# Kernel optimization log

Measured on AMD Instinct MI355X. Metric: run time of the kernel, lower is better.

## Reference

```python
import jax, jax.numpy as jnp
import numpy as np

N, DIN, DOUT = 8192, 256, 128
NEG_SLOPE = 0.01         # F.leaky_relu default
MASK_VAL = -9.0e15       # from the torch source


def setup_inputs() -> dict:
    key = jax.random.key(0)
    kx, kadj, kW, kbW, ka1, ka2, kba = jax.random.split(key, 7)
    x = jax.random.normal(kx, (N, DIN), dtype=jnp.float32)
    adj = jax.random.randint(kadj, (N, N), 0, 2, dtype=jnp.int32)
    # Linear W: input_dim -> output_dim
    W = jax.random.normal(kW, (DIN, DOUT), dtype=jnp.float32) * (1.0 / np.sqrt(DIN))
    bW = jax.random.normal(kbW, (DOUT,), dtype=jnp.float32) * 0.01
    # Linear a: 2*output_dim -> 1, split into the h_i part (a1) and h_j part (a2)
    a1 = jax.random.normal(ka1, (DOUT,), dtype=jnp.float32) * (1.0 / np.sqrt(2 * DOUT))
    a2 = jax.random.normal(ka2, (DOUT,), dtype=jnp.float32) * (1.0 / np.sqrt(2 * DOUT))
    ba = jax.random.normal(kba, (), dtype=jnp.float32) * 0.01
    return {"x": x, "adj": adj, "W": W, "bW": bW, "a1": a1, "a2": a2, "ba": ba}


def reference(x, adj, W, bW, a1, a2, ba):
    # h = W x + b  -> [N, DOUT]
    h = x @ W + bW
    # e[i,j] = leaky_relu(a . [h_i, h_j] + ba) = leaky_relu(a1.h_i + a2.h_j + ba)
    s_src = h @ a1            # [N]
    s_dst = h @ a2            # [N]
    e = s_src[:, None] + s_dst[None, :] + ba   # [N, N]
    e = jnp.where(e > 0, e, NEG_SLOPE * e)
    # mask non-edges, row softmax over neighbors j
    e = jnp.where(adj > 0, e, MASK_VAL)
    alpha = jax.nn.softmax(e, axis=1)          # [N, N]
    # dropout is identity in eval mode (dropout_rate=0)
    return alpha @ h                            # [N, DOUT]
```

## Files before the change

kernel.cpp:

```cpp
#include <hip/hip_runtime.h>
#include <hip/hip_bf16.h>


#define NN 8192
#define DIN 256
#define DOUT 128
#define LOG2E 1.4426950408889634f

typedef __attribute__((ext_vector_type(8))) short short8;
typedef __attribute__((ext_vector_type(4))) float floatx4;

__global__ void prep_wt(const float* __restrict__ W, __hip_bfloat16* __restrict__ WT) {
    int e = blockIdx.x * blockDim.x + threadIdx.x;
    if (e < DIN * DOUT) {
        int k = e >> 7;
        int d = e & 127;
        WT[d * DIN + k] = __float2bfloat16(W[e]);
    }
}

__global__ __launch_bounds__(256, 4) void gat_h(
    const float* __restrict__ x, const __hip_bfloat16* __restrict__ WT,
    const float* __restrict__ bW, const float* __restrict__ a1, const float* __restrict__ a2,
    __hip_bfloat16* __restrict__ hbT, float* __restrict__ s_src, float* __restrict__ s_dst) {
    int tid = threadIdx.x;
    int w = tid >> 6, lane = tid & 63;
    int lm = lane & 15, lq = lane >> 4;
    int i0 = blockIdx.x * 32;
    int r0 = (w >> 1) * 16;
    int c0 = (w & 1) * 64;

    __shared__ float s1s[32], s2s[32];
    if (tid < 32) { s1s[tid] = 0.f; s2s[tid] = 0.f; }
    __syncthreads();

    floatx4 acc[4] = {};
#pragma unroll
    for (int kk = 0; kk < DIN; kk += 32) {
        const float4* xp = (const float4*)&x[(size_t)(i0 + r0 + lm) * DIN + kk + lq * 8];
        float4 xa = xp[0], xb = xp[1];
        union { short8 v; __hip_bfloat16 h[8]; } af;
        af.h[0] = __float2bfloat16(xa.x); af.h[1] = __float2bfloat16(xa.y);
        af.h[2] = __float2bfloat16(xa.z); af.h[3] = __float2bfloat16(xa.w);
        af.h[4] = __float2bfloat16(xb.x); af.h[5] = __float2bfloat16(xb.y);
        af.h[6] = __float2bfloat16(xb.z); af.h[7] = __float2bfloat16(xb.w);
#pragma unroll
        for (int t = 0; t < 4; t++) {
            int d = c0 + 16 * t + lm;
            short8 bf = *(const short8*)&WT[(size_t)d * DIN + kk + lq * 8];
            acc[t] = __builtin_amdgcn_mfma_f32_16x16x32_bf16(af.v, bf, acc[t], 0, 0, 0);
        }
    }
    float s1[4] = {0.f, 0.f, 0.f, 0.f}, s2[4] = {0.f, 0.f, 0.f, 0.f};
#pragma unroll
    for (int t = 0; t < 4; t++) {
        int d = c0 + 16 * t + lm;
        float A1 = a1[d], A2 = a2[d], B = bW[d];
#pragma unroll
        for (int r = 0; r < 4; r++) {
            int row = r0 + lq * 4 + r;
            float h = acc[t][r] + B;
            hbT[(size_t)d * NN + i0 + row] = __float2bfloat16(h);
            s1[r] += h * A1;
            s2[r] += h * A2;
        }
    }
#pragma unroll
    for (int r = 0; r < 4; r++) {
        for (int m = 1; m < 16; m <<= 1) {
            s1[r] += __shfl_xor(s1[r], m, 64);
            s2[r] += __shfl_xor(s2[r], m, 64);
        }
    }
    if (lm == 0) {
#pragma unroll
        for (int r = 0; r < 4; r++) {
            int row = r0 + lq * 4 + r;
            atomicAdd(&s1s[row], s1[r]);
            atomicAdd(&s2s[row], s2[r]);
        }
    }
    __syncthreads();
    if (tid < 32) {
        s_src[i0 + tid] = s1s[tid] * LOG2E;
        s_dst[i0 + tid] = s2s[tid] * LOG2E;
    }
}

template <int NJT>
__global__ __launch_bounds__(256, 4) void gat_attn(
    const int* __restrict__ adj, const float* __restrict__ s_src,
    const float* __restrict__ s_dst, const float* __restrict__ ba_p,
    const __hip_bfloat16* __restrict__ hbT,
    float* __restrict__ num, float* __restrict__ lpart) {
    int tid = threadIdx.x;
    int w = tid >> 6, lane = tid & 63;
    int lm = lane & 15, lq = lane >> 4;
    int b = blockIdx.x;
    int ib = b & 127;
    int jh = b >> 7;
    int i0 = ib * 64 + w * 16;
    int jb0 = jh * (NJT * 32);

    const int* arow = adj + (size_t)(i0 + lm) * NN + jb0 + lq * 8;
    unsigned int mreg[NJT / 4];
#pragma unroll
    for (int t = 0; t < NJT; t++) {
        const int4* ap = (const int4*)(arow + t * 32);
        int4 v0 = ap[0], v1 = ap[1];
        unsigned int bb = 0;
        bb |= (v0.x != 0) ? 1u : 0u;
        bb |= (v0.y != 0) ? 2u : 0u;
        bb |= (v0.z != 0) ? 4u : 0u;
        bb |= (v0.w != 0) ? 8u : 0u;
        bb |= (v1.x != 0) ? 16u : 0u;
        bb |= (v1.y != 0) ? 32u : 0u;
        bb |= (v1.z != 0) ? 64u : 0u;
        bb |= (v1.w != 0) ? 128u : 0u;
        if ((t & 3) == 0) mreg[t >> 2] = bb;
        else              mreg[t >> 2] |= bb << ((t & 3) * 8);
    }

    float ssi = s_src[i0 + lm] + ba_p[0] * LOG2E;
    const float* sd = s_dst + jb0 + lq * 8;
    const __hip_bfloat16* hbb = hbT + (size_t)lm * NN + jb0 + lq * 8;

    floatx4 acc[8] = {};
    floatx4 accd = {};
    const short8 ones = { 0x3F80, 0x3F80, 0x3F80, 0x3F80, 0x3F80, 0x3F80, 0x3F80, 0x3F80 };

#pragma unroll
    for (int t = 0; t < NJT; t++) {
        unsigned int cm = (mreg[t >> 2] >> ((t & 3) * 8)) & 0xFFu;
        float4 cd0 = *(const float4*)(sd + t * 32);
        float4 cd1 = *(const float4*)(sd + t * 32 + 4);
        float p[8];
        {
            float e;
            e = ssi + cd0.x; e = fmaxf(e, 0.01f * e); p[0] = (cm & 1u)   ? __builtin_amdgcn_exp2f(e) : 0.f;
            e = ssi + cd0.y; e = fmaxf(e, 0.01f * e); p[1] = (cm & 2u)   ? __builtin_amdgcn_exp2f(e) : 0.f;
            e = ssi + cd0.z; e = fmaxf(e, 0.01f * e); p[2] = (cm & 4u)   ? __builtin_amdgcn_exp2f(e) : 0.f;
            e = ssi + cd0.w; e = fmaxf(e, 0.01f * e); p[3] = (cm & 8u)   ? __builtin_amdgcn_exp2f(e) : 0.f;
            e = ssi + cd1.x; e = fmaxf(e, 0.01f * e); p[4] = (cm & 16u)  ? __builtin_amdgcn_exp2f(e) : 0.f;
            e = ssi + cd1.y; e = fmaxf(e, 0.01f * e); p[5] = (cm & 32u)  ? __builtin_amdgcn_exp2f(e) : 0.f;
            e = ssi + cd1.z; e = fmaxf(e, 0.01f * e); p[6] = (cm & 64u)  ? __builtin_amdgcn_exp2f(e) : 0.f;
            e = ssi + cd1.w; e = fmaxf(e, 0.01f * e); p[7] = (cm & 128u) ? __builtin_amdgcn_exp2f(e) : 0.f;
        }
        union { short8 v; __hip_bfloat162 q[4]; } af;
        af.q[0] = __float22bfloat162_rn(make_float2(p[0], p[1]));
        af.q[1] = __float22bfloat162_rn(make_float2(p[2], p[3]));
        af.q[2] = __float22bfloat162_rn(make_float2(p[4], p[5]));
        af.q[3] = __float22bfloat162_rn(make_float2(p[6], p[7]));

        size_t off = (size_t)t * 32;
#pragma unroll
        for (int f = 0; f < 8; f++) {
            short8 bf = *(const short8*)(hbb + (size_t)f * 16 * NN + off);
            acc[f] = __builtin_amdgcn_mfma_f32_16x16x32_bf16(af.v, bf, acc[f], 0, 0, 0);
        }
        accd = __builtin_amdgcn_mfma_f32_16x16x32_bf16(af.v, ones, accd, 0, 0, 0);
    }

    float* nb = num + ((size_t)jh * NN + i0) * DOUT;
#pragma unroll
    for (int f = 0; f < 8; f++)
#pragma unroll
        for (int r = 0; r < 4; r++)
            nb[(size_t)(lq * 4 + r) * DOUT + f * 16 + lm] = acc[f][r];
    if (lm == 0) {
#pragma unroll
        for (int r = 0; r < 4; r++)
            lpart[(size_t)jh * NN + i0 + lq * 4 + r] = accd[r];
    }
}

__global__ void gat_combine(const float* __restrict__ num, const float* __restrict__ lpart,
                            float* __restrict__ out, int jsplit) {
    int gid = blockIdx.x * blockDim.x + threadIdx.x;
    int idx = gid * 4;
    int i = idx >> 7;
    float den = 0.f;
    for (int s = 0; s < jsplit; s++) den += lpart[(size_t)s * NN + i];
    float inv = 1.0f / den;
    float4 o = make_float4(0.f, 0.f, 0.f, 0.f);
    for (int s = 0; s < jsplit; s++) {
        float4 n = *(const float4*)&num[(size_t)s * NN * DOUT + idx];
        o.x += n.x; o.y += n.y; o.z += n.z; o.w += n.w;
    }
    o.x *= inv; o.y *= inv; o.z *= inv; o.w *= inv;
    *(float4*)&out[idx] = o;
}

extern "C" void kernel_launch(void* const* d_in, const int* in_sizes, int n_in,
                              void* d_out, int out_size, void* d_ws, size_t ws_size,
                              hipStream_t stream) {
    const float* x  = (const float*)d_in[0];
    const int* adj  = (const int*)d_in[1];
    const float* W  = (const float*)d_in[2];
    const float* bW = (const float*)d_in[3];
    const float* a1 = (const float*)d_in[4];
    const float* a2 = (const float*)d_in[5];
    const float* ba = (const float*)d_in[6];
    float* out = (float*)d_out;

    char* ws = (char*)d_ws;
    __hip_bfloat16* hbT  = (__hip_bfloat16*)ws;
    __hip_bfloat16* WT   = (__hip_bfloat16*)(ws + 2097152);
    float* s_src         = (float*)(ws + 2162688);
    float* s_dst         = (float*)(ws + 2195456);
    float* lpart         = (float*)(ws + 2228224);
    float* num           = (float*)(ws + 2490368);

    int jsplit = (ws_size >= 2490368 + (size_t)8 * NN * DOUT * 4) ? 8 : 4;

    prep_wt<<<128, 256, 0, stream>>>(W, WT);
    gat_h<<<256, 256, 0, stream>>>(x, WT, bW, a1, a2, hbT, s_src, s_dst);
    if (jsplit == 8)
        gat_attn<32><<<1024, 256, 0, stream>>>(adj, s_src, s_dst, ba, hbT, num, lpart);
    else
        gat_attn<64><<<512, 256, 0, stream>>>(adj, s_src, s_dst, ba, hbT, num, lpart);
    gat_combine<<<1024, 256, 0, stream>>>(num, lpart, out, jsplit);
}
```

Baseline: 504.1 us.

## Precompute packed adjacency bitmask in a separate kernel before attention

Adds a build_mask kernel that converts the int32 adjacency matrix into a byte-per-8-columns bitmask, stored in a layout permuted so each attention lane can fetch its mask bytes with wide vector loads. The attention kernel then reads the compact mask instead of streaming the int32 adjacency rows itself. The aim is better-coalesced reading of the large adjacency matrix and less load pressure inside the MFMA loop. It costs an extra launch and an extra mask round trip, removes overlap of adjacency loading with compute, and needs a larger workspace, which could force the smaller split.

```diff
diff --git a/kernel.cpp b/kernel.cpp
--- a/kernel.cpp
+++ b/kernel.cpp
@@ -88,8 +88,27 @@
 }
 
 template <int NJT>
+__global__ void build_mask(const int* __restrict__ adj, unsigned char* __restrict__ mask) {
+    size_t gid = (size_t)blockIdx.x * blockDim.x + threadIdx.x;
+    const int4* a = (const int4*)(adj + gid * 8);
+    int4 v0 = a[0], v1 = a[1];
+    unsigned int b = 0;
+    b |= (v0.x != 0) ? 1u : 0u;
+    b |= (v0.y != 0) ? 2u : 0u;
+    b |= (v0.z != 0) ? 4u : 0u;
+    b |= (v0.w != 0) ? 8u : 0u;
+    b |= (v1.x != 0) ? 16u : 0u;
+    b |= (v1.y != 0) ? 32u : 0u;
+    b |= (v1.z != 0) ? 64u : 0u;
+    b |= (v1.w != 0) ? 128u : 0u;
+    unsigned int g = (unsigned int)gid & (NJT * 4 - 1);
+    size_t pos = (gid & ~(size_t)(NJT * 4 - 1)) | ((g & 3) * NJT + (g >> 2));
+    mask[pos] = (unsigned char)b;
+}
+
+template <int NJT>
 __global__ __launch_bounds__(256, 4) void gat_attn(
-    const int* __restrict__ adj, const float* __restrict__ s_src,
+    const unsigned char* __restrict__ mask, const float* __restrict__ s_src,
     const float* __restrict__ s_dst, const float* __restrict__ ba_p,
     const __hip_bfloat16* __restrict__ hbT,
     float* __restrict__ num, float* __restrict__ lpart) {
@@ -102,24 +121,10 @@
     int i0 = ib * 64 + w * 16;
     int jb0 = jh * (NJT * 32);
 
-    const int* arow = adj + (size_t)(i0 + lm) * NN + jb0 + lq * 8;
-    unsigned int mreg[NJT / 4];
-#pragma unroll
-    for (int t = 0; t < NJT; t++) {
-        const int4* ap = (const int4*)(arow + t * 32);
-        int4 v0 = ap[0], v1 = ap[1];
-        unsigned int bb = 0;
-        bb |= (v0.x != 0) ? 1u : 0u;
-        bb |= (v0.y != 0) ? 2u : 0u;
-        bb |= (v0.z != 0) ? 4u : 0u;
-        bb |= (v0.w != 0) ? 8u : 0u;
-        bb |= (v1.x != 0) ? 16u : 0u;
-        bb |= (v1.y != 0) ? 32u : 0u;
-        bb |= (v1.z != 0) ? 64u : 0u;
-        bb |= (v1.w != 0) ? 128u : 0u;
-        if ((t & 3) == 0) mreg[t >> 2] = bb;
-        else              mreg[t >> 2] |= bb << ((t & 3) * 8);
-    }
+    const unsigned char* mrow = mask + (size_t)(i0 + lm) * (NN / 8) + jh * (NJT * 4) + lq * NJT;
+    union { uint4 v[NJT / 16]; unsigned int u[NJT / 4]; } mr;
+#pragma unroll
+    for (int q = 0; q < NJT / 16; q++) mr.v[q] = ((const uint4*)mrow)[q];
 
     float ssi = s_src[i0 + lm] + ba_p[0] * LOG2E;
     const float* sd = s_dst + jb0 + lq * 8;
@@ -131,7 +136,7 @@
 
 #pragma unroll
     for (int t = 0; t < NJT; t++) {
-        unsigned int cm = (mreg[t >> 2] >> ((t & 3) * 8)) & 0xFFu;
+        unsigned int cm = (mr.u[t >> 2] >> ((t & 3) * 8)) & 0xFFu;
         float4 cd0 = *(const float4*)(sd + t * 32);
         float4 cd1 = *(const float4*)(sd + t * 32 + 4);
         float p[8];
@@ -209,15 +214,19 @@
     float* s_src         = (float*)(ws + 2162688);
     float* s_dst         = (float*)(ws + 2195456);
     float* lpart         = (float*)(ws + 2228224);
-    float* num           = (float*)(ws + 2490368);
-
-    int jsplit = (ws_size >= 2490368 + (size_t)8 * NN * DOUT * 4) ? 8 : 4;
+    unsigned char* mask  = (unsigned char*)(ws + 2490368);
+    float* num           = (float*)(ws + 10878976);
+
+    int jsplit = (ws_size >= 10878976 + (size_t)8 * NN * DOUT * 4) ? 8 : 4;
 
     prep_wt<<<128, 256, 0, stream>>>(W, WT);
     gat_h<<<256, 256, 0, stream>>>(x, WT, bW, a1, a2, hbT, s_src, s_dst);
-    if (jsplit == 8)
-        gat_attn<32><<<1024, 256, 0, stream>>>(adj, s_src, s_dst, ba, hbT, num, lpart);
-    else
-        gat_attn<64><<<512, 256, 0, stream>>>(adj, s_src, s_dst, ba, hbT, num, lpart);
+    if (jsplit == 8) {
+        build_mask<32><<<32768, 256, 0, stream>>>(adj, mask);
+        gat_attn<32><<<1024, 256, 0, stream>>>(mask, s_src, s_dst, ba, hbT, num, lpart);
+    } else {
+        build_mask<64><<<32768, 256, 0, stream>>>(adj, mask);
+        gat_attn<64><<<512, 256, 0, stream>>>(mask, s_src, s_dst, ba, hbT, num, lpart);
+    }
     gat_combine<<<1024, 256, 0, stream>>>(num, lpart, out, jsplit);
 }
```

Result: no change. 509.6 us (+1.1%).
